# Kernel tuning notes

Hardware: AMD Instinct MI355X
Metric: run time of the kernel (lower is better)

The kernel has to match this reference:

```python
import jax, jax.numpy as jnp
import numpy as np

B, IN, HS = 4096, 1024, 1024


def setup_inputs() -> dict:
    key = jax.random.key(0)
    ks = jax.random.split(key, 20)
    inp = {
        "x": jax.random.normal(ks[0], (B, IN), jnp.float32),
        "h": jax.random.normal(ks[1], (B, HS), jnp.float32),
        "c": jax.random.normal(ks[2], (B, HS), jnp.float32),
    }
    names_x = ["Wix", "Wfx", "Wgx", "Wox"]
    names_h = ["Wih", "Wfh", "Wgh", "Woh"]
    bnames_x = ["bix", "bfx", "bgx", "box"]
    bnames_h = ["bih", "bfh", "bgh", "boh"]
    k = 3
    for wn, bn in zip(names_x, bnames_x):
        inp[wn] = jax.random.normal(ks[k], (HS, IN), jnp.float32) * 0.02; k += 1
        inp[bn] = jax.random.normal(ks[k], (HS,), jnp.float32) * 0.02; k += 1
    for wn, bn in zip(names_h, bnames_h):
        inp[wn] = jax.random.normal(ks[k], (HS, HS), jnp.float32) * 0.02; k += 1
        inp[bn] = jax.random.normal(ks[k], (HS,), jnp.float32) * 0.02; k += 1
    return inp


def reference(x, h, c,
              Wix, bix, Wfx, bfx, Wgx, bgx, Wox, box,
              Wih, bih, Wfh, bfh, Wgh, bgh, Woh, boh):
    # torch Linear: y = x @ W.T + b
    i = jax.nn.sigmoid(x @ Wix.T + bix + h @ Wih.T + bih)
    f = jax.nn.sigmoid(x @ Wfx.T + bfx + h @ Wfh.T + bfh)
    g = jnp.tanh(x @ Wgx.T + bgx + h @ Wgh.T + bgh)
    o = jax.nn.sigmoid(x @ Wox.T + box + h @ Woh.T + boh)
    c_new = f * c + i * g
    h_new = o * jnp.tanh(c_new)
    return (h_new, c_new)
```

## Files before the change

### kernel.cpp

```cpp
#include <hip/hip_runtime.h>
#include <hip/hip_bf16.h>
#include <stdint.h>

#define BATCH  4096
#define IN_DIM 1024
#define HS     1024
#define K_DIM  2048
#define N_DIM  4096
#define BK 64
#define NKT (K_DIM / BK)
#define HALF_BYTES 16384
#define TPB_BYTES  (NKT * HALF_BYTES)

typedef __bf16 bf16x8 __attribute__((ext_vector_type(8)));
typedef float  f32x4  __attribute__((ext_vector_type(4)));

__device__ __forceinline__ unsigned short f2bf(float f) {
    union { float f; uint32_t u; } a; a.f = f;
    uint32_t r = a.u + 0x7FFF + ((a.u >> 16) & 1);
    return (unsigned short)(r >> 16);
}
__device__ __forceinline__ uint32_t pk2(float a, float b) {
    return (uint32_t)f2bf(a) | ((uint32_t)f2bf(b) << 16);
}

__device__ __forceinline__ void load16_lds(const void* g, void* l) {
    __builtin_amdgcn_global_load_lds(
        (const __attribute__((address_space(1))) uint32_t*)g,
        (__attribute__((address_space(3))) uint32_t*)(uintptr_t)l,
        16, 0, 0);
}
__device__ __forceinline__ void stage16k(const char* g, char* l, int wid, int lane) {
    load16_lds(g + wid * 1024 + lane * 16,        l + wid * 1024);
    load16_lds(g + 8192 + wid * 1024 + lane * 16, l + 8192 + wid * 1024);
}

__device__ __forceinline__ float sigf(float x)  { return 1.0f / (1.0f + __expf(-x)); }
__device__ __forceinline__ float tanhf_(float x){ return 1.0f - 2.0f / (__expf(2.0f * x) + 1.0f); }

#define BAR()   __builtin_amdgcn_s_barrier()
#define PRIO(x) __builtin_amdgcn_s_setprio(x)
#define VMC0()  asm volatile("s_waitcnt vmcnt(0)" ::: "memory")

__device__ __forceinline__ void rdA4(bf16x8 (&d)[4], const char* base, int kb0, int kb1) {
    d[0] = *(const bf16x8*)(base + kb0);
    d[1] = *(const bf16x8*)(base + kb1);
    d[2] = *(const bf16x8*)(base + 2048 + kb0);
    d[3] = *(const bf16x8*)(base + 2048 + kb1);
}
__device__ __forceinline__ void rdB8(bf16x8 (&d)[8], const char* base, int kb0, int kb1) {
    #pragma unroll
    for (int j = 0; j < 4; ++j) {
        d[j]     = *(const bf16x8*)(base + j * 2048 + kb0);
        d[4 + j] = *(const bf16x8*)(base + j * 2048 + kb1);
    }
}
template<int Q>
__device__ __forceinline__ void mfq(f32x4 (&acc)[8][4], const bf16x8 (&a)[4],
                                    const bf16x8 (&b)[8]) {
    #pragma unroll
    for (int mf = 0; mf < 2; ++mf)
        #pragma unroll
        for (int ks = 0; ks < 2; ++ks)
            #pragma unroll
            for (int j = 0; j < 4; ++j)
                acc[2 * Q + mf][j] = __builtin_amdgcn_mfma_f32_16x16x32_bf16(
                    a[mf * 2 + ks], b[ks * 4 + j], acc[2 * Q + mf][j], 0, 0, 0);
}

__global__ void pack_kernel(const float* __restrict__ x, const float* __restrict__ h,
                            const float* __restrict__ Wix, const float* __restrict__ Wfx,
                            const float* __restrict__ Wgx, const float* __restrict__ Wox,
                            const float* __restrict__ Wih, const float* __restrict__ Wfh,
                            const float* __restrict__ Wgh, const float* __restrict__ Woh,
                            uint4* __restrict__ Apk, uint4* __restrict__ Bpk)
{
    int t = blockIdx.x * blockDim.x + threadIdx.x;
    const int NCHUNK = (BATCH * K_DIM) / 8;
    bool isB = t >= NCHUNK;
    int ci = isB ? (t - NCHUNK) : t;

    int cb  = ci & 7;
    int row = (ci >> 3) & 127;
    int kt  = (ci >> 10) & 31;
    int bt  = ci >> 15;

    int k0 = kt * BK + ((cb ^ (row & 7)) << 3);
    int gr = bt * 128 + row;

    const float* src;
    if (!isB) {
        src = (k0 < IN_DIM) ? (x + (size_t)gr * IN_DIM + k0)
                            : (h + (size_t)gr * HS + (k0 - IN_DIM));
    } else {
        int q = (gr >> 4) & 3;
        int u = ((gr >> 6) << 4) | (gr & 15);
        const float* Wq = (k0 < IN_DIM)
            ? ((q == 0) ? Wix : (q == 1) ? Wfx : (q == 2) ? Wgx : Wox)
            : ((q == 0) ? Wih : (q == 1) ? Wfh : (q == 2) ? Wgh : Woh);
        int kk = (k0 < IN_DIM) ? k0 : (k0 - IN_DIM);
        src = Wq + (size_t)u * 1024 + kk;
    }
    float4 v0 = ((const float4*)src)[0];
    float4 v1 = ((const float4*)src)[1];
    uint4 o;
    o.x = pk2(v0.x, v0.y); o.y = pk2(v0.z, v0.w);
    o.z = pk2(v1.x, v1.y); o.w = pk2(v1.z, v1.w);
    (isB ? Bpk : Apk)[ci] = o;
}

__global__ void __launch_bounds__(512, 2)
gemm_kernel(const char* __restrict__ Apk, const char* __restrict__ Bpk,
            const float* __restrict__ c,
            const float* __restrict__ bix, const float* __restrict__ bfx,
            const float* __restrict__ bgx, const float* __restrict__ box_,
            const float* __restrict__ bih, const float* __restrict__ bfh,
            const float* __restrict__ bgh, const float* __restrict__ boh,
            float* __restrict__ out)
{
    __shared__ uint4 lds4[131072 / 16];
    char* lds = (char*)lds4;

    const int tid  = threadIdx.x;
    const int lane = tid & 63;
    const int wid  = tid >> 6;
    const int wm   = wid >> 2;
    const int wn   = wid & 3;
    const int fr   = lane & 15;
    const int kg   = lane >> 4;

    const int phys = blockIdx.x;
    const int virt = (phys & 7) * 32 + (phys >> 3);
    const int bn   = virt & 15;
    const int bm   = virt >> 4;

    const char* gA = Apk + (size_t)(bm * 2) * TPB_BYTES;
    const char* gB = Bpk + (size_t)(bn * 2) * TPB_BYTES;

    const int kb0   = (kg * 16) ^ ((fr & 7) << 4);
    const int kb1   = kb0 ^ 64;
    const int aOff  = wm * 16384 + fr * 128;
    const int bOff  = 32768 + wn * 8192 + fr * 128;

    f32x4 acc[8][4] = {};
    bf16x8 a0[4], a1[4], a2[4], a3[4], bC[8];

    stage16k(gA + (size_t)(0 * NKT + 0) * HALF_BYTES, lds + 0,     wid, lane);
    stage16k(gA + (size_t)(1 * NKT + 0) * HALF_BYTES, lds + 16384, wid, lane);
    stage16k(gB + (size_t)(0 * NKT + 0) * HALF_BYTES, lds + 32768, wid, lane);
    stage16k(gB + (size_t)(1 * NKT + 0) * HALF_BYTES, lds + 49152, wid, lane);

    for (int t = 0; t < NKT - 1; ++t) {
        char* L  = lds + (t & 1) * 65536;
        char* Ln = lds + ((t & 1) ^ 1) * 65536;
        VMC0();
        BAR();
        stage16k(gA + (size_t)(0 * NKT + t + 1) * HALF_BYTES, Ln + 0,     wid, lane);
        stage16k(gA + (size_t)(1 * NKT + t + 1) * HALF_BYTES, Ln + 16384, wid, lane);
        stage16k(gB + (size_t)(0 * NKT + t + 1) * HALF_BYTES, Ln + 32768, wid, lane);
        stage16k(gB + (size_t)(1 * NKT + t + 1) * HALF_BYTES, Ln + 49152, wid, lane);
        rdB8(bC, L + bOff, kb0, kb1);
        rdA4(a0, L + aOff,         kb0, kb1);
        rdA4(a1, L + aOff + 4096,  kb0, kb1);
        PRIO(1); mfq<0>(acc, a0, bC); PRIO(0);
        rdA4(a2, L + aOff + 8192,  kb0, kb1);
        PRIO(1); mfq<1>(acc, a1, bC); PRIO(0);
        rdA4(a3, L + aOff + 12288, kb0, kb1);
        PRIO(1); mfq<2>(acc, a2, bC); PRIO(0);
        PRIO(1); mfq<3>(acc, a3, bC); PRIO(0);
    }

    const int u  = bn * 64 + wn * 16 + fr;
    const int r0 = bm * 256 + wm * 128;
    {
        char* L = lds + ((NKT - 1) & 1) * 65536;
        VMC0();
        BAR();
        float cpre[8][4];
        #pragma unroll
        for (int ai = 0; ai < 8; ++ai) {
            const int rowb = r0 + ai * 16 + kg * 4;
            #pragma unroll
            for (int r = 0; r < 4; ++r)
                cpre[ai][r] = c[(size_t)(rowb + r) * HS + u];
        }
        const float bi = bix[u] + bih[u];
        const float bf = bfx[u] + bfh[u];
        const float bg = bgx[u] + bgh[u];
        const float bo = box_[u] + boh[u];

        rdB8(bC, L + bOff, kb0, kb1);
        rdA4(a0, L + aOff,         kb0, kb1);
        rdA4(a1, L + aOff + 4096,  kb0, kb1);
        PRIO(1); mfq<0>(acc, a0, bC); PRIO(0);
        rdA4(a2, L + aOff + 8192,  kb0, kb1);
        PRIO(1); mfq<1>(acc, a1, bC); PRIO(0);
        rdA4(a3, L + aOff + 12288, kb0, kb1);
        PRIO(1); mfq<2>(acc, a2, bC); PRIO(0);
        PRIO(1); mfq<3>(acc, a3, bC); PRIO(0);

        float* hout = out;
        float* cout = out + (size_t)BATCH * HS;
        #pragma unroll
        for (int ai = 0; ai < 8; ++ai) {
            const int rowb = r0 + ai * 16 + kg * 4;
            #pragma unroll
            for (int r = 0; r < 4; ++r) {
                const size_t idx = (size_t)(rowb + r) * HS + u;
                float iv = sigf  (acc[ai][0][r] + bi);
                float fv = sigf  (acc[ai][1][r] + bf);
                float gv = tanhf_(acc[ai][2][r] + bg);
                float ov = sigf  (acc[ai][3][r] + bo);
                float cn = fv * cpre[ai][r] + iv * gv;
                hout[idx] = ov * tanhf_(cn);
                cout[idx] = cn;
            }
        }
    }
}

extern "C" void kernel_launch(void* const* d_in, const int* in_sizes, int n_in,
                              void* d_out, int out_size, void* d_ws, size_t ws_size,
                              hipStream_t stream)
{
    const float* x   = (const float*)d_in[0];
    const float* h   = (const float*)d_in[1];
    const float* c   = (const float*)d_in[2];
    const float* Wix = (const float*)d_in[3];  const float* bix = (const float*)d_in[4];
    const float* Wfx = (const float*)d_in[5];  const float* bfx = (const float*)d_in[6];
    const float* Wgx = (const float*)d_in[7];  const float* bgx = (const float*)d_in[8];
    const float* Wox = (const float*)d_in[9];  const float* box_ = (const float*)d_in[10];
    const float* Wih = (const float*)d_in[11]; const float* bih = (const float*)d_in[12];
    const float* Wfh = (const float*)d_in[13]; const float* bfh = (const float*)d_in[14];
    const float* Wgh = (const float*)d_in[15]; const float* bgh = (const float*)d_in[16];
    const float* Woh = (const float*)d_in[17]; const float* boh = (const float*)d_in[18];

    char* ws = (char*)d_ws;
    uint4* Apk = (uint4*)ws;
    uint4* Bpk = (uint4*)(ws + (size_t)16 * 1024 * 1024);

    pack_kernel<<<8192, 256, 0, stream>>>(x, h, Wix, Wfx, Wgx, Wox,
                                          Wih, Wfh, Wgh, Woh, Apk, Bpk);
    gemm_kernel<<<256, 512, 0, stream>>>((const char*)Apk, (const char*)Bpk, c,
                                         bix, bfx, bgx, box_, bih, bfh, bgh, boh,
                                         (float*)d_out);
}
```

Measured before the change: 95.06 us.

## Load B fragments directly to registers and triple-buffer A tiles in LDS

The B (weight) operand is no longer staged through LDS. Each wave loads its B fragments straight from global memory into double-buffered registers, and the packing kernel drops the swizzle for B to match. The A operand moves to a three-stage LDS ring with prefetch distance two and partial vmcnt waits, and LDS shrinks from 128KB to 96KB. The aim is to cut LDS traffic and barrier stalls, at the cost of more registers and uncoalesced-looking global B loads that each wave repeats.

```diff
diff --git a/kernel.cpp b/kernel.cpp
--- a/kernel.cpp
+++ b/kernel.cpp
@@ -39,8 +39,9 @@
 __device__ __forceinline__ float tanhf_(float x){ return 1.0f - 2.0f / (__expf(2.0f * x) + 1.0f); }
 
 #define BAR()   __builtin_amdgcn_s_barrier()
+#define DSB()   __builtin_amdgcn_sched_barrier(0)
 #define PRIO(x) __builtin_amdgcn_s_setprio(x)
-#define VMC0()  asm volatile("s_waitcnt vmcnt(0)" ::: "memory")
+#define VMC(n)  asm volatile("s_waitcnt vmcnt(" #n ")" ::: "memory")
 
 __device__ __forceinline__ void rdA4(bf16x8 (&d)[4], const char* base, int kb0, int kb1) {
     d[0] = *(const bf16x8*)(base + kb0);
@@ -48,12 +49,12 @@
     d[2] = *(const bf16x8*)(base + 2048 + kb0);
     d[3] = *(const bf16x8*)(base + 2048 + kb1);
 }
-__device__ __forceinline__ void rdB8(bf16x8 (&d)[8], const char* base, int kb0, int kb1) {
+__device__ __forceinline__ void loadB8(bf16x8 (&d)[8], const char* p) {
     #pragma unroll
-    for (int j = 0; j < 4; ++j) {
-        d[j]     = *(const bf16x8*)(base + j * 2048 + kb0);
-        d[4 + j] = *(const bf16x8*)(base + j * 2048 + kb1);
-    }
+    for (int ks = 0; ks < 2; ++ks)
+        #pragma unroll
+        for (int j = 0; j < 4; ++j)
+            d[ks * 4 + j] = *(const bf16x8*)(p + j * 2048 + ks * 64);
 }
 template<int Q>
 __device__ __forceinline__ void mfq(f32x4 (&acc)[8][4], const bf16x8 (&a)[4],
@@ -85,14 +86,14 @@
     int kt  = (ci >> 10) & 31;
     int bt  = ci >> 15;
 
-    int k0 = kt * BK + ((cb ^ (row & 7)) << 3);
     int gr = bt * 128 + row;
-
     const float* src;
     if (!isB) {
+        int k0 = kt * BK + ((cb ^ (row & 7)) << 3);
         src = (k0 < IN_DIM) ? (x + (size_t)gr * IN_DIM + k0)
                             : (h + (size_t)gr * HS + (k0 - IN_DIM));
     } else {
+        int k0 = kt * BK + (cb << 3);
         int q = (gr >> 4) & 3;
         int u = ((gr >> 6) << 4) | (gr & 15);
         const float* Wq = (k0 < IN_DIM)
@@ -118,7 +119,7 @@
             const float* __restrict__ bgh, const float* __restrict__ boh,
             float* __restrict__ out)
 {
-    __shared__ uint4 lds4[131072 / 16];
+    __shared__ uint4 lds4[98304 / 16];
     char* lds = (char*)lds4;
 
     const int tid  = threadIdx.x;
@@ -135,47 +136,60 @@
     const int bm   = virt >> 4;
 
     const char* gA = Apk + (size_t)(bm * 2) * TPB_BYTES;
-    const char* gB = Bpk + (size_t)(bn * 2) * TPB_BYTES;
-
-    const int kb0   = (kg * 16) ^ ((fr & 7) << 4);
-    const int kb1   = kb0 ^ 64;
-    const int aOff  = wm * 16384 + fr * 128;
-    const int bOff  = 32768 + wn * 8192 + fr * 128;
+    const char* gBW = Bpk + (size_t)(bn * 2 + (wn >> 1)) * TPB_BYTES
+                    + ((wn & 1) * 64 + fr) * 128 + kg * 16;
+
+    const int kb0  = (kg * 16) ^ ((fr & 7) << 4);
+    const int kb1  = kb0 ^ 64;
+    const int aOff = wm * 16384 + fr * 128;
 
     f32x4 acc[8][4] = {};
-    bf16x8 a0[4], a1[4], a2[4], a3[4], bC[8];
-
-    stage16k(gA + (size_t)(0 * NKT + 0) * HALF_BYTES, lds + 0,     wid, lane);
-    stage16k(gA + (size_t)(1 * NKT + 0) * HALF_BYTES, lds + 16384, wid, lane);
-    stage16k(gB + (size_t)(0 * NKT + 0) * HALF_BYTES, lds + 32768, wid, lane);
-    stage16k(gB + (size_t)(1 * NKT + 0) * HALF_BYTES, lds + 49152, wid, lane);
-
-    for (int t = 0; t < NKT - 1; ++t) {
-        char* L  = lds + (t & 1) * 65536;
-        char* Ln = lds + ((t & 1) ^ 1) * 65536;
-        VMC0();
-        BAR();
-        stage16k(gA + (size_t)(0 * NKT + t + 1) * HALF_BYTES, Ln + 0,     wid, lane);
-        stage16k(gA + (size_t)(1 * NKT + t + 1) * HALF_BYTES, Ln + 16384, wid, lane);
-        stage16k(gB + (size_t)(0 * NKT + t + 1) * HALF_BYTES, Ln + 32768, wid, lane);
-        stage16k(gB + (size_t)(1 * NKT + t + 1) * HALF_BYTES, Ln + 49152, wid, lane);
-        rdB8(bC, L + bOff, kb0, kb1);
-        rdA4(a0, L + aOff,         kb0, kb1);
-        rdA4(a1, L + aOff + 4096,  kb0, kb1);
-        PRIO(1); mfq<0>(acc, a0, bC); PRIO(0);
-        rdA4(a2, L + aOff + 8192,  kb0, kb1);
-        PRIO(1); mfq<1>(acc, a1, bC); PRIO(0);
-        rdA4(a3, L + aOff + 12288, kb0, kb1);
-        PRIO(1); mfq<2>(acc, a2, bC); PRIO(0);
-        PRIO(1); mfq<3>(acc, a3, bC); PRIO(0);
-    }
+    bf16x8 a0[4], a1[4], a2[4], a3[4], bU[8], bV[8];
+
+    loadB8(bU, gBW + (size_t)0 * HALF_BYTES);
+    DSB();
+    stage16k(gA + (size_t)0 * HALF_BYTES,             lds + 0,             wid, lane);
+    stage16k(gA + TPB_BYTES + (size_t)0 * HALF_BYTES, lds + 16384,         wid, lane);
+    stage16k(gA + (size_t)1 * HALF_BYTES,             lds + 32768,         wid, lane);
+    stage16k(gA + TPB_BYTES + (size_t)1 * HALF_BYTES, lds + 32768 + 16384, wid, lane);
+    VMC(4);
+    BAR();
+
+#define GTILE(T, BCUR, BNXT, LDB, STG, VMCN)                                  \
+    {                                                                         \
+      const int t_ = (T);                                                     \
+      char* L  = lds + (t_ % 3) * 32768;                                      \
+      if (LDB) loadB8(BNXT, gBW + (size_t)(t_ + 1) * HALF_BYTES);             \
+      DSB();                                                                  \
+      if (STG) {                                                              \
+        char* Ls = lds + ((t_ + 2) % 3) * 32768;                              \
+        stage16k(gA + (size_t)(t_ + 2) * HALF_BYTES,             Ls,         wid, lane); \
+        stage16k(gA + TPB_BYTES + (size_t)(t_ + 2) * HALF_BYTES, Ls + 16384, wid, lane); \
+      }                                                                       \
+      DSB();                                                                  \
+      rdA4(a0, L + aOff,         kb0, kb1);                                   \
+      rdA4(a1, L + aOff + 4096,  kb0, kb1);                                   \
+      PRIO(1); mfq<0>(acc, a0, BCUR); PRIO(0);                                \
+      rdA4(a2, L + aOff + 8192,  kb0, kb1);                                   \
+      PRIO(1); mfq<1>(acc, a1, BCUR); PRIO(0);                                \
+      rdA4(a3, L + aOff + 12288, kb0, kb1);                                   \
+      PRIO(1); mfq<2>(acc, a2, BCUR); PRIO(0);                                \
+      PRIO(1); mfq<3>(acc, a3, BCUR); PRIO(0);                                \
+      VMC(VMCN);                                                              \
+      BAR();                                                                  \
+    }
+
+    for (int t = 0; t < NKT - 2; t += 2) {
+        GTILE(t,     bU, bV, true, t     + 2 < NKT, 12);
+        GTILE(t + 1, bV, bU, true, t + 1 + 2 < NKT, 12);
+    }
+    GTILE(NKT - 2, bU, bV, true, false, 8);
+#undef GTILE
 
     const int u  = bn * 64 + wn * 16 + fr;
     const int r0 = bm * 256 + wm * 128;
     {
-        char* L = lds + ((NKT - 1) & 1) * 65536;
-        VMC0();
-        BAR();
+        char* L = lds + ((NKT - 1) % 3) * 32768;
         float cpre[8][4];
         #pragma unroll
         for (int ai = 0; ai < 8; ++ai) {
@@ -189,15 +203,14 @@
         const float bg = bgx[u] + bgh[u];
         const float bo = box_[u] + boh[u];
 
-        rdB8(bC, L + bOff, kb0, kb1);
         rdA4(a0, L + aOff,         kb0, kb1);
         rdA4(a1, L + aOff + 4096,  kb0, kb1);
-        PRIO(1); mfq<0>(acc, a0, bC); PRIO(0);
+        PRIO(1); mfq<0>(acc, a0, bV); PRIO(0);
         rdA4(a2, L + aOff + 8192,  kb0, kb1);
-        PRIO(1); mfq<1>(acc, a1, bC); PRIO(0);
+        PRIO(1); mfq<1>(acc, a1, bV); PRIO(0);
         rdA4(a3, L + aOff + 12288, kb0, kb1);
-        PRIO(1); mfq<2>(acc, a2, bC); PRIO(0);
-        PRIO(1); mfq<3>(acc, a3, bC); PRIO(0);
+        PRIO(1); mfq<2>(acc, a2, bV); PRIO(0);
+        PRIO(1); mfq<3>(acc, a3, bV); PRIO(0);
 
         float* hout = out;
         float* cout = out + (size_t)BATCH * HS;
```

Result: slower. 130.5 us (+37.2%).
